# Kernel tuning notes

Measured on AMD Instinct MI355X. Metric: run time of the kernel, lower is better.

Reference implementation:

```python
import jax, jax.numpy as jnp
import numpy as np

N_NODES = 50000
N_EDGES = 800000
IN_C, HID_C, OUT_C = 128, 128, 64


def setup_inputs() -> dict:
    key = jax.random.key(0)
    k1, k2, k3, k4 = jax.random.split(key, 4)
    x = jax.random.normal(k1, (N_NODES, IN_C), dtype=jnp.float32)
    edge_index = jax.random.randint(k2, (2, N_EDGES), 0, N_NODES, dtype=jnp.int64)
    # Glorot-ish init for weights, zero bias (PyG GCNConv default has bias)
    W1 = jax.random.normal(k3, (IN_C, HID_C), dtype=jnp.float32) * (1.0 / np.sqrt(IN_C))
    b1 = jnp.zeros((HID_C,), dtype=jnp.float32)
    W2 = jax.random.normal(k4, (HID_C, OUT_C), dtype=jnp.float32) * (1.0 / np.sqrt(HID_C))
    b2 = jnp.zeros((OUT_C,), dtype=jnp.float32)
    return {"x": x, "edge_index": edge_index, "W1": W1, "b1": b1, "W2": W2, "b2": b2}


def _gcn_norm(edge_index, num_nodes):
    """PyG gcn_norm: add self-loops, symmetric deg^{-1/2} normalization."""
    loop = jnp.arange(num_nodes, dtype=edge_index.dtype)
    src = jnp.concatenate([edge_index[0], loop])  # [E + N]
    dst = jnp.concatenate([edge_index[1], loop])
    ones = jnp.ones(src.shape[0], dtype=jnp.float32)
    deg = jax.ops.segment_sum(ones, dst, num_segments=num_nodes)  # in-degree incl. self-loop
    dinv = jnp.where(deg > 0, jax.lax.rsqrt(deg), 0.0)
    norm = dinv[src] * dinv[dst]  # [E + N]
    return src, dst, norm


def _gcn_conv(x, W, b, src, dst, norm, num_nodes):
    h = x @ W                                   # [N, C_out] transform first (PyG order)
    msg = h[src] * norm[:, None]                # gather + normalize, [E+N, C_out]
    out = jax.ops.segment_sum(msg, dst, num_segments=num_nodes)  # scatter-add
    return out + b


def reference(x, edge_index, W1, b1, W2, b2):
    N = x.shape[0]
    src, dst, norm = _gcn_norm(edge_index, N)  # graph normalization shared by both layers
    h = jax.nn.relu(_gcn_conv(x, W1, b1, src, dst, norm, N))
    out = _gcn_conv(h, W2, b2, src, dst, norm, N)
    return out
```

## Files before the change

kernel.cpp:

```cpp
#include <hip/hip_runtime.h>
#include <hip/hip_bf16.h>

#define IN_C  128
#define HID_C 128
#define OUT_CC 64
#define BK    128
#define CAPLG 12

using short8  = __attribute__((ext_vector_type(8))) short;
using float4v = __attribute__((ext_vector_type(4))) float;

__device__ __forceinline__ unsigned short f2b(float f) {
    unsigned int u = __float_as_uint(f);
    return (unsigned short)((u + 0x7fffu + ((u >> 16) & 1u)) >> 16);
}
__device__ __forceinline__ unsigned int pack2(float a, float b) {
    return (unsigned int)f2b(a) | ((unsigned int)f2b(b) << 16);
}
__device__ __forceinline__ float2 bf2_to_f2(unsigned int v) {
    float2 r;
    r.x = __uint_as_float(v << 16);
    r.y = __uint_as_float(v & 0xffff0000u);
    return r;
}


__global__ __launch_bounds__(256) void k_setup(const float* __restrict__ W1,
                                               const float* __restrict__ W2,
                                               const int* __restrict__ ei,
                                               unsigned short* __restrict__ w1f,
                                               unsigned short* __restrict__ w2f,
                                               int* __restrict__ flag,
                                               int* __restrict__ bfill, int NBK) {
    int e = blockIdx.x * 256 + threadIdx.x;
    if (e < 16384) {
        int j = e & 7, lane = (e >> 3) & 63, ks = (e >> 9) & 3, nt = e >> 11;
        int k = ks * 32 + ((lane >> 4) << 3) + j;
        int n = nt * 16 + (lane & 15);
        w1f[e] = f2b(W1[k * 128 + n]);
    } else if (e < 16384 + 8192) {
        int e2 = e - 16384;
        int j = e2 & 7, lane = (e2 >> 3) & 63, ks = (e2 >> 9) & 3, nt = e2 >> 11;
        int k = ks * 32 + ((lane >> 4) << 3) + j;
        int n = nt * 16 + (lane & 15);
        w2f[e2] = f2b(W2[k * 64 + n]);
    }
    if (blockIdx.x == 0) {
        for (int i = threadIdx.x; i < NBK; i += 256) bfill[i] = 0;
        if (threadIdx.x == 0) {
            int odd_zero = 1, any_even = 0;
            for (int i = 0; i < 64; ++i) {
                if (ei[2 * i + 1] != 0) odd_zero = 0;
                if (ei[2 * i] != 0) any_even = 1;
            }
            *flag = (odd_zero && any_even) ? 2 : 1;
        }
    }
}

__global__ __launch_bounds__(256) void k_bpart(const int* __restrict__ ei,
                                               const int* __restrict__ flag,
                                               int* __restrict__ bfill,
                                               int* __restrict__ ebuf, int E, int NBK) {
    __shared__ int lh[512];
    __shared__ int lbase[512];
    const int t = threadIdx.x;
    for (int i = t; i < NBK; i += 256) lh[i] = 0;
    __syncthreads();
    const int st = *flag;
    const int base = blockIdx.x * 2048;
    int s[8], d[8];
    #pragma unroll
    for (int j = 0; j < 8; ++j) {
        int i = base + j * 256 + t;
        if (i < E) {
            s[j] = ei[(size_t)st * i];
            d[j] = ei[(size_t)st * ((size_t)E + i)];
            atomicAdd(&lh[d[j] >> 7], 1);
        } else d[j] = -1;
    }
    __syncthreads();
    for (int i = t; i < NBK; i += 256) {
        int c = lh[i];
        lbase[i] = c ? atomicAdd(&bfill[i], c) : 0;
        lh[i] = 0;
    }
    __syncthreads();
    #pragma unroll
    for (int j = 0; j < 8; ++j) {
        if (d[j] >= 0) {
            int b = d[j] >> 7;
            int r = lbase[b] + atomicAdd(&lh[b], 1);
            if (r < (1 << CAPLG))
                ebuf[(b << CAPLG) + r] = s[j] | ((d[j] & (BK - 1)) << 20);
        }
    }
}

__global__ __launch_bounds__(256) void k_blmg1(const int* __restrict__ ebuf,
                                               const int* __restrict__ bfill,
                                               int2* __restrict__ begend,
                                               float* __restrict__ dinv,
                                               int* __restrict__ col,
                                               const float* __restrict__ x,
                                               const unsigned short* __restrict__ w1f,
                                               unsigned short* __restrict__ h,
                                               int N, int NBK) {
    __shared__ unsigned short lds[64 * 136];
    const int t = threadIdx.x;

    if ((int)blockIdx.x < NBK) {
        int* cnt = (int*)lds;
        int* sc  = cnt + BK;
        int* off = sc + BK;
        const int n0 = blockIdx.x * BK;
        const int beg = (int)blockIdx.x << CAPLG;
        const int ecnt = min(bfill[blockIdx.x], 1 << CAPLG);
        if (t < BK) cnt[t] = 0;
        __syncthreads();
        for (int i = t; i < ecnt; i += 256)
            atomicAdd(&cnt[ebuf[beg + i] >> 20], 1);
        __syncthreads();
        if (t < BK) sc[t] = cnt[t];
        __syncthreads();
        for (int o = 1; o < BK; o <<= 1) {
            int v = (t < BK && t >= o) ? sc[t - o] : 0;
            __syncthreads();
            if (t < BK) sc[t] += v;
            __syncthreads();
        }
        if (t < BK) {
            int c = cnt[t];
            off[t] = sc[t] - c;
            if (n0 + t < N) {
                begend[n0 + t] = make_int2(beg + off[t], beg + sc[t]);
                dinv[n0 + t] = rsqrtf((float)c + 1.0f);
            }
            cnt[t] = 0;
        }
        __syncthreads();
        for (int i = t; i < ecnt; i += 256) {
            int e = ebuf[beg + i];
            int dl = e >> 20;
            int p = beg + off[dl] + atomicAdd(&cnt[dl], 1);
            col[p] = e & 0xFFFFF;
        }
        return;
    }

    const int row0 = ((int)blockIdx.x - NBK) * 64;
    {
        int r = t >> 2, cc = (t & 3) * 32;
        int grow = row0 + r;
        unsigned int* dst = (unsigned int*)&lds[r * 136 + cc];
        if (grow < N) {
            const float4* src = (const float4*)(x + (size_t)grow * 128 + cc);
            #pragma unroll
            for (int i = 0; i < 8; ++i) {
                float4 v = src[i];
                dst[2 * i]     = pack2(v.x, v.y);
                dst[2 * i + 1] = pack2(v.z, v.w);
            }
        } else {
            #pragma unroll
            for (int i = 0; i < 16; ++i) dst[i] = 0;
        }
    }
    __syncthreads();
    const int w = t >> 6, lane = t & 63;
    const int quad = lane >> 4, m = lane & 15;
    short8 a[4];
    #pragma unroll
    for (int ks = 0; ks < 4; ++ks)
        a[ks] = *(const short8*)&lds[(w * 16 + m) * 136 + ks * 32 + quad * 8];
    float4v acc[8];
    #pragma unroll
    for (int nt = 0; nt < 8; ++nt) acc[nt] = (float4v){0.f, 0.f, 0.f, 0.f};
    const short8* wf = (const short8*)w1f;
    #pragma unroll
    for (int nt = 0; nt < 8; ++nt)
        #pragma unroll
        for (int ks = 0; ks < 4; ++ks)
            acc[nt] = __builtin_amdgcn_mfma_f32_16x16x32_bf16(a[ks], wf[(nt * 4 + ks) * 64 + lane],
                                                              acc[nt], 0, 0, 0);
    #pragma unroll
    for (int nt = 0; nt < 8; ++nt)
        #pragma unroll
        for (int r = 0; r < 4; ++r) {
            int grow = row0 + w * 16 + quad * 4 + r;
            if (grow < N) h[(size_t)grow * 128 + nt * 16 + m] = f2b(acc[nt][r]);
        }
}

__global__ __launch_bounds__(256) void k_agg128e(const uint4* __restrict__ feat,
                                                 const int2* __restrict__ begend,
                                                 const int* __restrict__ col,
                                                 const float* __restrict__ dinv,
                                                 const float* __restrict__ b1,
                                                 uint4* __restrict__ h1b, int N) {
    const int grp = threadIdx.x >> 4;
    const int l16 = threadIdx.x & 15;
    const int node = blockIdx.x * 16 + grp;
    if (node >= N) return;
    const float dd = dinv[node];
    const int2 be = begend[node];
    const int beg = be.x, end = be.y;
    float a0, a1, a2, a3, a4, a5, a6, a7;
    {
        uint4 sv = feat[(size_t)node * 16 + l16];
        float2 q;
        q = bf2_to_f2(sv.x); a0 = q.x * dd; a1 = q.y * dd;
        q = bf2_to_f2(sv.y); a2 = q.x * dd; a3 = q.y * dd;
        q = bf2_to_f2(sv.z); a4 = q.x * dd; a5 = q.y * dd;
        q = bf2_to_f2(sv.w); a6 = q.x * dd; a7 = q.y * dd;
    }
    int e = beg;
    for (; e + 4 <= end; e += 4) {
        int s0 = col[e], s1 = col[e + 1], s2 = col[e + 2], s3 = col[e + 3];
        float w0 = dinv[s0], w1 = dinv[s1], w2 = dinv[s2], w3 = dinv[s3];
        uint4 u0 = feat[(size_t)s0 * 16 + l16];
        uint4 u1 = feat[(size_t)s1 * 16 + l16];
        uint4 u2 = feat[(size_t)s2 * 16 + l16];
        uint4 u3 = feat[(size_t)s3 * 16 + l16];
        float2 q;
        q = bf2_to_f2(u0.x); a0 += q.x * w0; a1 += q.y * w0;
        q = bf2_to_f2(u0.y); a2 += q.x * w0; a3 += q.y * w0;
        q = bf2_to_f2(u0.z); a4 += q.x * w0; a5 += q.y * w0;
        q = bf2_to_f2(u0.w); a6 += q.x * w0; a7 += q.y * w0;
        q = bf2_to_f2(u1.x); a0 += q.x * w1; a1 += q.y * w1;
        q = bf2_to_f2(u1.y); a2 += q.x * w1; a3 += q.y * w1;
        q = bf2_to_f2(u1.z); a4 += q.x * w1; a5 += q.y * w1;
        q = bf2_to_f2(u1.w); a6 += q.x * w1; a7 += q.y * w1;
        q = bf2_to_f2(u2.x); a0 += q.x * w2; a1 += q.y * w2;
        q = bf2_to_f2(u2.y); a2 += q.x * w2; a3 += q.y * w2;
        q = bf2_to_f2(u2.z); a4 += q.x * w2; a5 += q.y * w2;
        q = bf2_to_f2(u2.w); a6 += q.x * w2; a7 += q.y * w2;
        q = bf2_to_f2(u3.x); a0 += q.x * w3; a1 += q.y * w3;
        q = bf2_to_f2(u3.y); a2 += q.x * w3; a3 += q.y * w3;
        q = bf2_to_f2(u3.z); a4 += q.x * w3; a5 += q.y * w3;
        q = bf2_to_f2(u3.w); a6 += q.x * w3; a7 += q.y * w3;
    }
    for (; e < end; ++e) {
        int s = col[e];
        float w = dinv[s];
        uint4 u = feat[(size_t)s * 16 + l16];
        float2 q;
        q = bf2_to_f2(u.x); a0 += q.x * w; a1 += q.y * w;
        q = bf2_to_f2(u.y); a2 += q.x * w; a3 += q.y * w;
        q = bf2_to_f2(u.z); a4 += q.x * w; a5 += q.y * w;
        q = bf2_to_f2(u.w); a6 += q.x * w; a7 += q.y * w;
    }
    float4 ba = ((const float4*)b1)[2 * l16];
    float4 bb = ((const float4*)b1)[2 * l16 + 1];
    a0 = fmaxf(a0 * dd + ba.x, 0.0f);
    a1 = fmaxf(a1 * dd + ba.y, 0.0f);
    a2 = fmaxf(a2 * dd + ba.z, 0.0f);
    a3 = fmaxf(a3 * dd + ba.w, 0.0f);
    a4 = fmaxf(a4 * dd + bb.x, 0.0f);
    a5 = fmaxf(a5 * dd + bb.y, 0.0f);
    a6 = fmaxf(a6 * dd + bb.z, 0.0f);
    a7 = fmaxf(a7 * dd + bb.w, 0.0f);
    uint4 o;
    o.x = pack2(a0, a1);
    o.y = pack2(a2, a3);
    o.z = pack2(a4, a5);
    o.w = pack2(a6, a7);
    h1b[(size_t)node * 16 + l16] = o;
}

__global__ __launch_bounds__(256) void k_mg2(const unsigned int* __restrict__ h1b,
                                             const unsigned short* __restrict__ w2f,
                                             unsigned short* __restrict__ h2, int N) {
    __shared__ unsigned short lds[64 * 136];
    const int t = threadIdx.x;
    const int row0 = blockIdx.x * 64;
    {
        int r = t >> 2, cc = (t & 3) * 32;
        int grow = row0 + r;
        uint4* dst = (uint4*)&lds[r * 136 + cc];
        if (grow < N) {
            const uint4* src = (const uint4*)(h1b + (size_t)grow * 64 + (cc >> 1));
            #pragma unroll
            for (int i = 0; i < 4; ++i) dst[i] = src[i];
        } else {
            #pragma unroll
            for (int i = 0; i < 4; ++i) dst[i] = (uint4){0, 0, 0, 0};
        }
    }
    __syncthreads();
    const int w = t >> 6, lane = t & 63;
    const int quad = lane >> 4, m = lane & 15;
    short8 a[4];
    #pragma unroll
    for (int ks = 0; ks < 4; ++ks)
        a[ks] = *(const short8*)&lds[(w * 16 + m) * 136 + ks * 32 + quad * 8];
    float4v acc[4];
    #pragma unroll
    for (int nt = 0; nt < 4; ++nt) acc[nt] = (float4v){0.f, 0.f, 0.f, 0.f};
    const short8* wf = (const short8*)w2f;
    #pragma unroll
    for (int nt = 0; nt < 4; ++nt)
        #pragma unroll
        for (int ks = 0; ks < 4; ++ks)
            acc[nt] = __builtin_amdgcn_mfma_f32_16x16x32_bf16(a[ks], wf[(nt * 4 + ks) * 64 + lane],
                                                              acc[nt], 0, 0, 0);
    #pragma unroll
    for (int nt = 0; nt < 4; ++nt)
        #pragma unroll
        for (int r = 0; r < 4; ++r) {
            int grow = row0 + w * 16 + quad * 4 + r;
            if (grow < N) h2[(size_t)grow * 64 + nt * 16 + m] = f2b(acc[nt][r]);
        }
}

__global__ __launch_bounds__(256) void k_agg64(const uint2* __restrict__ feat,
                                               const int2* __restrict__ begend,
                                               const int* __restrict__ col,
                                               const float* __restrict__ dinv,
                                               const float* __restrict__ bias,
                                               float* __restrict__ out, int N) {
    const int grp = threadIdx.x >> 4;
    const int l16 = threadIdx.x & 15;
    const int node = blockIdx.x * 16 + grp;
    if (node >= N) return;
    const float dd = dinv[node];
    const int2 be = begend[node];
    const int beg = be.x, end = be.y;
    float a0, a1, a2, a3;
    {
        uint2 sv = feat[(size_t)node * 16 + l16];
        float2 q;
        q = bf2_to_f2(sv.x); a0 = q.x * dd; a1 = q.y * dd;
        q = bf2_to_f2(sv.y); a2 = q.x * dd; a3 = q.y * dd;
    }
    int e = beg;
    for (; e + 4 <= end; e += 4) {
        int s0 = col[e], s1 = col[e + 1], s2 = col[e + 2], s3 = col[e + 3];
        float w0 = dinv[s0], w1 = dinv[s1], w2 = dinv[s2], w3 = dinv[s3];
        uint2 u0 = feat[(size_t)s0 * 16 + l16];
        uint2 u1 = feat[(size_t)s1 * 16 + l16];
        uint2 u2 = feat[(size_t)s2 * 16 + l16];
        uint2 u3 = feat[(size_t)s3 * 16 + l16];
        float2 q;
        q = bf2_to_f2(u0.x); a0 += q.x * w0; a1 += q.y * w0;
        q = bf2_to_f2(u0.y); a2 += q.x * w0; a3 += q.y * w0;
        q = bf2_to_f2(u1.x); a0 += q.x * w1; a1 += q.y * w1;
        q = bf2_to_f2(u1.y); a2 += q.x * w1; a3 += q.y * w1;
        q = bf2_to_f2(u2.x); a0 += q.x * w2; a1 += q.y * w2;
        q = bf2_to_f2(u2.y); a2 += q.x * w2; a3 += q.y * w2;
        q = bf2_to_f2(u3.x); a0 += q.x * w3; a1 += q.y * w3;
        q = bf2_to_f2(u3.y); a2 += q.x * w3; a3 += q.y * w3;
    }
    for (; e < end; ++e) {
        int s = col[e];
        float w = dinv[s];
        uint2 u = feat[(size_t)s * 16 + l16];
        float2 q;
        q = bf2_to_f2(u.x); a0 += q.x * w; a1 += q.y * w;
        q = bf2_to_f2(u.y); a2 += q.x * w; a3 += q.y * w;
    }
    float4 b = ((const float4*)bias)[l16];
    float4 o;
    o.x = a0 * dd + b.x;
    o.y = a1 * dd + b.y;
    o.z = a2 * dd + b.z;
    o.w = a3 * dd + b.w;
    ((float4*)out)[(size_t)node * 16 + l16] = o;
}

extern "C" void kernel_launch(void* const* d_in, const int* in_sizes, int n_in,
                              void* d_out, int out_size, void* d_ws, size_t ws_size,
                              hipStream_t stream) {
    const float* x  = (const float*)d_in[0];
    const int*   ei = (const int*)d_in[1];
    const float* W1 = (const float*)d_in[2];
    const float* b1 = (const float*)d_in[3];
    const float* W2 = (const float*)d_in[4];
    const float* b2 = (const float*)d_in[5];

    const int N = in_sizes[0] / IN_C;
    const int E = in_sizes[1] / 2;
    const int NBK  = (N + BK - 1) / BK;
    const int NCHK = (E + 2047) / 2048;
    const int NT1  = (N + 63) / 64;

    char* ws = (char*)d_ws;
    int*            flag    = (int*)(ws + 0);
    int*            bfill   = (int*)(ws + 64);
    int2*           begend  = (int2*)(ws + 4096);
    float*          dinv    = (float*)(ws + 404480);
    unsigned short* w1f     = (unsigned short*)(ws + 604672);
    unsigned short* w2f     = (unsigned short*)(ws + 637440);
    int*            ebuf    = (int*)(ws + 655360);
    int*            col     = (int*)(ws + 7061504);
    unsigned short* h       = (unsigned short*)(ws + 13467904);
    uint4*          h1b     = (uint4*)(ws + 26267904);

    k_setup<<<96, 256, 0, stream>>>(W1, W2, ei, w1f, w2f, flag, bfill, NBK);

    k_bpart<<<NCHK, 256, 0, stream>>>(ei, flag, bfill, ebuf, E, NBK);

    k_blmg1<<<NBK + NT1, 256, 0, stream>>>(ebuf, bfill, begend, dinv, col,
                                           x, w1f, h, N, NBK);

    k_agg128e<<<(N + 15) / 16, 256, 0, stream>>>((const uint4*)h, begend, col, dinv, b1, h1b, N);

    unsigned short* h2 = h;
    k_mg2<<<NT1, 256, 0, stream>>>((const unsigned int*)h1b, w2f, h2, N);
    k_agg64<<<(N + 15) / 16, 256, 0, stream>>>((const uint2*)h2, begend, col, dinv, b2, (float*)d_out, N);
}
```

Before: 172.4 us.

## Co-schedule edge bucket partitioning with first GEMM, split local CSR build out

The GEMM-1 blocks (x @ W1) now run in the same launch as the edge bucket-partition blocks instead of alongside the per-bucket CSR build. The per-bucket local sort, degree and offset computation moves into its own kernel that runs afterwards. The aim is to overlap the bandwidth-heavy edge scatter with the compute-bound MFMA transform. Launch count stays the same, but the lighter local-sort kernel now runs alone instead of overlapping with the GEMM.

```diff
diff --git a/kernel.cpp b/kernel.cpp
--- a/kernel.cpp
+++ b/kernel.cpp
@@ -58,97 +58,54 @@
     }
 }
 
-__global__ __launch_bounds__(256) void k_bpart(const int* __restrict__ ei,
+__global__ __launch_bounds__(256) void k_bpmg1(const int* __restrict__ ei,
                                                const int* __restrict__ flag,
                                                int* __restrict__ bfill,
-                                               int* __restrict__ ebuf, int E, int NBK) {
-    __shared__ int lh[512];
-    __shared__ int lbase[512];
-    const int t = threadIdx.x;
-    for (int i = t; i < NBK; i += 256) lh[i] = 0;
-    __syncthreads();
-    const int st = *flag;
-    const int base = blockIdx.x * 2048;
-    int s[8], d[8];
-    #pragma unroll
-    for (int j = 0; j < 8; ++j) {
-        int i = base + j * 256 + t;
-        if (i < E) {
-            s[j] = ei[(size_t)st * i];
-            d[j] = ei[(size_t)st * ((size_t)E + i)];
-            atomicAdd(&lh[d[j] >> 7], 1);
-        } else d[j] = -1;
-    }
-    __syncthreads();
-    for (int i = t; i < NBK; i += 256) {
-        int c = lh[i];
-        lbase[i] = c ? atomicAdd(&bfill[i], c) : 0;
-        lh[i] = 0;
-    }
-    __syncthreads();
-    #pragma unroll
-    for (int j = 0; j < 8; ++j) {
-        if (d[j] >= 0) {
-            int b = d[j] >> 7;
-            int r = lbase[b] + atomicAdd(&lh[b], 1);
-            if (r < (1 << CAPLG))
-                ebuf[(b << CAPLG) + r] = s[j] | ((d[j] & (BK - 1)) << 20);
-        }
-    }
-}
-
-__global__ __launch_bounds__(256) void k_blmg1(const int* __restrict__ ebuf,
-                                               const int* __restrict__ bfill,
-                                               int2* __restrict__ begend,
-                                               float* __restrict__ dinv,
-                                               int* __restrict__ col,
+                                               int* __restrict__ ebuf,
                                                const float* __restrict__ x,
                                                const unsigned short* __restrict__ w1f,
                                                unsigned short* __restrict__ h,
-                                               int N, int NBK) {
+                                               int E, int N, int NBK, int NCHK) {
     __shared__ unsigned short lds[64 * 136];
     const int t = threadIdx.x;
 
-    if ((int)blockIdx.x < NBK) {
-        int* cnt = (int*)lds;
-        int* sc  = cnt + BK;
-        int* off = sc + BK;
-        const int n0 = blockIdx.x * BK;
-        const int beg = (int)blockIdx.x << CAPLG;
-        const int ecnt = min(bfill[blockIdx.x], 1 << CAPLG);
-        if (t < BK) cnt[t] = 0;
+    if ((int)blockIdx.x < NCHK) {
+        int* lh    = (int*)lds;
+        int* lbase = lh + 512;
+        for (int i = t; i < NBK; i += 256) lh[i] = 0;
         __syncthreads();
-        for (int i = t; i < ecnt; i += 256)
-            atomicAdd(&cnt[ebuf[beg + i] >> 20], 1);
+        const int st = *flag;
+        const int base = blockIdx.x * 2048;
+        int s[8], d[8];
+        #pragma unroll
+        for (int j = 0; j < 8; ++j) {
+            int i = base + j * 256 + t;
+            if (i < E) {
+                s[j] = ei[(size_t)st * i];
+                d[j] = ei[(size_t)st * ((size_t)E + i)];
+                atomicAdd(&lh[d[j] >> 7], 1);
+            } else d[j] = -1;
+        }
         __syncthreads();
-        if (t < BK) sc[t] = cnt[t];
+        for (int i = t; i < NBK; i += 256) {
+            int c = lh[i];
+            lbase[i] = c ? atomicAdd(&bfill[i], c) : 0;
+            lh[i] = 0;
+        }
         __syncthreads();
-        for (int o = 1; o < BK; o <<= 1) {
-            int v = (t < BK && t >= o) ? sc[t - o] : 0;
-            __syncthreads();
-            if (t < BK) sc[t] += v;
-            __syncthreads();
-        }
-        if (t < BK) {
-            int c = cnt[t];
-            off[t] = sc[t] - c;
-            if (n0 + t < N) {
-                begend[n0 + t] = make_int2(beg + off[t], beg + sc[t]);
-                dinv[n0 + t] = rsqrtf((float)c + 1.0f);
+        #pragma unroll
+        for (int j = 0; j < 8; ++j) {
+            if (d[j] >= 0) {
+                int b = d[j] >> 7;
+                int r = lbase[b] + atomicAdd(&lh[b], 1);
+                if (r < (1 << CAPLG))
+                    ebuf[(b << CAPLG) + r] = s[j] | ((d[j] & (BK - 1)) << 20);
             }
-            cnt[t] = 0;
-        }
-        __syncthreads();
-        for (int i = t; i < ecnt; i += 256) {
-            int e = ebuf[beg + i];
-            int dl = e >> 20;
-            int p = beg + off[dl] + atomicAdd(&cnt[dl], 1);
-            col[p] = e & 0xFFFFF;
         }
         return;
     }
 
-    const int row0 = ((int)blockIdx.x - NBK) * 64;
+    const int row0 = ((int)blockIdx.x - NCHK) * 64;
     {
         int r = t >> 2, cc = (t & 3) * 32;
         int grow = row0 + r;
@@ -190,6 +147,49 @@
             int grow = row0 + w * 16 + quad * 4 + r;
             if (grow < N) h[(size_t)grow * 128 + nt * 16 + m] = f2b(acc[nt][r]);
         }
+}
+
+__global__ __launch_bounds__(256) void k_blocal(const int* __restrict__ ebuf,
+                                                const int* __restrict__ bfill,
+                                                int2* __restrict__ begend,
+                                                float* __restrict__ dinv,
+                                                int* __restrict__ col, int N) {
+    __shared__ int cnt[BK];
+    __shared__ int sc[BK];
+    __shared__ int off[BK];
+    const int t = threadIdx.x;
+    const int n0 = blockIdx.x * BK;
+    const int beg = (int)blockIdx.x << CAPLG;
+    const int ecnt = min(bfill[blockIdx.x], 1 << CAPLG);
+    if (t < BK) cnt[t] = 0;
+    __syncthreads();
+    for (int i = t; i < ecnt; i += 256)
+        atomicAdd(&cnt[ebuf[beg + i] >> 20], 1);
+    __syncthreads();
+    if (t < BK) sc[t] = cnt[t];
+    __syncthreads();
+    for (int o = 1; o < BK; o <<= 1) {
+        int v = (t < BK && t >= o) ? sc[t - o] : 0;
+        __syncthreads();
+        if (t < BK) sc[t] += v;
+        __syncthreads();
+    }
+    if (t < BK) {
+        int c = cnt[t];
+        off[t] = sc[t] - c;
+        if (n0 + t < N) {
+            begend[n0 + t] = make_int2(beg + off[t], beg + sc[t]);
+            dinv[n0 + t] = rsqrtf((float)c + 1.0f);
+        }
+        cnt[t] = 0;
+    }
+    __syncthreads();
+    for (int i = t; i < ecnt; i += 256) {
+        int e = ebuf[beg + i];
+        int dl = e >> 20;
+        int p = beg + off[dl] + atomicAdd(&cnt[dl], 1);
+        col[p] = e & 0xFFFFF;
+    }
 }
 
 __global__ __launch_bounds__(256) void k_agg128e(const uint4* __restrict__ feat,
@@ -398,10 +398,10 @@
 
     k_setup<<<96, 256, 0, stream>>>(W1, W2, ei, w1f, w2f, flag, bfill, NBK);
 
-    k_bpart<<<NCHK, 256, 0, stream>>>(ei, flag, bfill, ebuf, E, NBK);
-
-    k_blmg1<<<NBK + NT1, 256, 0, stream>>>(ebuf, bfill, begend, dinv, col,
-                                           x, w1f, h, N, NBK);
+    k_bpmg1<<<NCHK + NT1, 256, 0, stream>>>(ei, flag, bfill, ebuf, x, w1f, h,
+                                            E, N, NBK, NCHK);
+
+    k_blocal<<<NBK, 256, 0, stream>>>(ebuf, bfill, begend, dinv, col, N);
 
     k_agg128e<<<(N + 15) / 16, 256, 0, stream>>>((const uint4*)h, begend, col, dinv, b1, h1b, N);
 
```

After: 172.5 us. Within noise of the previous version (+0.1%).
